# Kernel tuning notes

Hardware: AMD Instinct MI355X
Metric: run time of the kernel (lower is better)

The kernel has to match this reference:

```python
import jax, jax.numpy as jnp
import numpy as np

UNITS = 1024
B, T, F = 32, 2048, 2048  # values: [B, T, F], key dim = F // 2
DQ = 1024                 # query feature dim


def setup_inputs() -> dict:
    key = jax.random.key(0)
    k1, k2, k3, k4 = jax.random.split(key, 4)
    query = jax.random.normal(k1, (B, DQ), dtype=jnp.float32)
    values = jax.random.normal(k2, (B, T, F), dtype=jnp.float32)
    concat_dim = F // 2 + DQ  # key half concat with repeated query
    W1 = jax.random.normal(k3, (concat_dim, UNITS), dtype=jnp.float32) * (concat_dim ** -0.5)
    b1 = jnp.zeros((UNITS,), dtype=jnp.float32)
    V = jax.random.normal(k4, (UNITS, 1), dtype=jnp.float32) * (UNITS ** -0.5)
    bV = jnp.zeros((1,), dtype=jnp.float32)
    return {"query": query, "values": values, "W1": W1, "b1": b1, "V": V, "bV": bV}


def reference(query, values, W1, b1, V, bV):
    half = values.shape[2] // 2
    key = values[:, :, :half]                       # [B, T, F/2]
    # RepeatVector(query) -> [B, T, DQ]; concat with key -> [B, T, F/2 + DQ]
    s_prev = jnp.broadcast_to(query[:, None, :], (values.shape[0], values.shape[1], query.shape[1]))
    concat = jnp.concatenate([key, s_prev], axis=-1)
    e = jnp.einsum('btc,cu->btu', concat, W1) + b1   # Dense(units), no activation
    score = jnp.einsum('btu,uo->bto', e, V) + bV     # [B, T, 1]
    attention_weights = jax.nn.softmax(score, axis=1)
    # Dot(axes=1): contract time axis -> [B, 1, F]
    context_vector = jnp.einsum('bto,btf->bof', attention_weights, values)
    return (context_vector, attention_weights)
```

## Files before the change

kernel.cpp:

```cpp
#include <hip/hip_runtime.h>
#include <math.h>

#define BB 32
#define TT 2048
#define FF 2048
#define DQ 1024
#define UNITS 1024
#define HALF 1024
#define CDIM 2048
#define TC 32
#define NC (TT / TC)


__global__ void compute_w_kernel(const float* __restrict__ W1,
                                 const float* __restrict__ b1,
                                 const float* __restrict__ V,
                                 const float* __restrict__ bV,
                                 float* __restrict__ ws_w,
                                 float* __restrict__ ws_c0) {
    int g = blockIdx.x * 4 + (threadIdx.x >> 6);
    int lane = threadIdx.x & 63;
    if (g > CDIM) return;
    const float* src = (g < CDIM) ? (W1 + (size_t)g * UNITS) : b1;
    float acc = 0.f;
#pragma unroll
    for (int k = 0; k < UNITS / 256; ++k) {
        int idx = k * 256 + lane * 4;
        float4 a = *(const float4*)(src + idx);
        float4 v = *(const float4*)(V + idx);
        acc += a.x * v.x + a.y * v.y + a.z * v.z + a.w * v.w;
    }
#pragma unroll
    for (int off = 32; off >= 1; off >>= 1) acc += __shfl_down(acc, off, 64);
    if (lane == 0) {
        if (g < CDIM) ws_w[g] = acc;
        else          *ws_c0 = acc + bV[0];
    }
}

__global__ void compute_qb_kernel(const float* __restrict__ query,
                                  const float* __restrict__ ws_w,
                                  const float* __restrict__ ws_c0,
                                  float* __restrict__ ws_qb) {
    int g = blockIdx.x * 4 + (threadIdx.x >> 6);
    int lane = threadIdx.x & 63;
    if (g >= BB) return;
    const float* q = query + (size_t)g * DQ;
    const float* wq = ws_w + HALF;
    float acc = 0.f;
#pragma unroll
    for (int k = 0; k < DQ / 256; ++k) {
        int idx = k * 256 + lane * 4;
        float4 a = *(const float4*)(q + idx);
        float4 w = *(const float4*)(wq + idx);
        acc += a.x * w.x + a.y * w.y + a.z * w.z + a.w * w.w;
    }
#pragma unroll
    for (int off = 32; off >= 1; off >>= 1) acc += __shfl_down(acc, off, 64);
    if (lane == 0) ws_qb[g] = acc + *ws_c0;
}

__global__ void attn_stream_kernel(const float* __restrict__ values,
                                   const float* __restrict__ ws_w,
                                   const float* __restrict__ ws_qb,
                                   float* __restrict__ ws_scores,
                                   float* __restrict__ ws_m,
                                   float* __restrict__ ws_l,
                                   float* __restrict__ ws_ctx) {
    const int blk = blockIdx.x;
    const int b = blk / NC;
    const int chunk = blk % NC;
    const int t0 = chunk * TC;
    const int tid = threadIdx.x;
    const int lane = tid & 63;
    const int wv = tid >> 6;

    __shared__ float red[16];

    const float4 w4 = *(const float4*)(ws_w + tid * 4);
    const float qb = ws_qb[b];

    const float* vbase = values + (size_t)b * TT * FF;

    float m = -1e30f, l = 0.f;
    float4 c0 = make_float4(0.f, 0.f, 0.f, 0.f);
    float4 c1 = make_float4(0.f, 0.f, 0.f, 0.f);

    for (int r = 0; r < TC; r += 2) {
        const float* row0 = vbase + (size_t)(t0 + r) * FF;
        const float* row1 = row0 + FF;
        float4 a0 = *(const float4*)(row0 + tid * 4);
        float4 a1 = *(const float4*)(row0 + HALF + tid * 4);
        float4 e0 = *(const float4*)(row1 + tid * 4);
        float4 e1 = *(const float4*)(row1 + HALF + tid * 4);

        float pa = a0.x * w4.x + a0.y * w4.y + a0.z * w4.z + a0.w * w4.w;
        float pb = e0.x * w4.x + e0.y * w4.y + e0.z * w4.z + e0.w * w4.w;
#pragma unroll
        for (int off = 32; off >= 1; off >>= 1) {
            pa += __shfl_down(pa, off, 64);
            pb += __shfl_down(pb, off, 64);
        }
        const int par = (r >> 1) & 1;
        if (lane == 0) {
            red[par * 8 + wv * 2 + 0] = pa;
            red[par * 8 + wv * 2 + 1] = pb;
        }
        __syncthreads();
        float sa = red[par * 8 + 0] + red[par * 8 + 2] + red[par * 8 + 4] + red[par * 8 + 6] + qb;
        float sb = red[par * 8 + 1] + red[par * 8 + 3] + red[par * 8 + 5] + red[par * 8 + 7] + qb;
        if (tid == 0) {
            ws_scores[b * TT + t0 + r]     = sa;
            ws_scores[b * TT + t0 + r + 1] = sb;
        }
        {
            float mn = fmaxf(m, sa);
            float scl = __expf(m - mn);
            float p = __expf(sa - mn);
            l = l * scl + p;
            c0.x = c0.x * scl + p * a0.x; c0.y = c0.y * scl + p * a0.y;
            c0.z = c0.z * scl + p * a0.z; c0.w = c0.w * scl + p * a0.w;
            c1.x = c1.x * scl + p * a1.x; c1.y = c1.y * scl + p * a1.y;
            c1.z = c1.z * scl + p * a1.z; c1.w = c1.w * scl + p * a1.w;
            m = mn;
        }
        {
            float mn = fmaxf(m, sb);
            float scl = __expf(m - mn);
            float p = __expf(sb - mn);
            l = l * scl + p;
            c0.x = c0.x * scl + p * e0.x; c0.y = c0.y * scl + p * e0.y;
            c0.z = c0.z * scl + p * e0.z; c0.w = c0.w * scl + p * e0.w;
            c1.x = c1.x * scl + p * e1.x; c1.y = c1.y * scl + p * e1.y;
            c1.z = c1.z * scl + p * e1.z; c1.w = c1.w * scl + p * e1.w;
            m = mn;
        }
    }

    if (tid == 0) { ws_m[blk] = m; ws_l[blk] = l; }
    float* cdst = ws_ctx + (size_t)blk * FF;
    *(float4*)(cdst + tid * 4) = c0;
    *(float4*)(cdst + HALF + tid * 4) = c1;
}

__global__ void combine_kernel(const float* __restrict__ ws_scores,
                               const float* __restrict__ ws_m,
                               const float* __restrict__ ws_l,
                               const float* __restrict__ ws_ctx,
                               float* __restrict__ out) {
    const int b = blockIdx.x >> 3;
    const int seg = blockIdx.x & 7;
    const int tid = threadIdx.x;

    __shared__ float ms[NC], ls[NC];
    for (int c = tid; c < NC; c += 256) {
        ms[c] = ws_m[b * NC + c];
        ls[c] = ws_l[b * NC + c];
    }
    __syncthreads();

    float mg = -1e30f;
#pragma unroll 8
    for (int c = 0; c < NC; ++c) mg = fmaxf(mg, ms[c]);
    float lg = 0.f;
#pragma unroll 8
    for (int c = 0; c < NC; ++c) lg += ls[c] * __expf(ms[c] - mg);
    const float inv = 1.0f / lg;

    const int t = seg * 256 + tid;
    float s = ws_scores[b * TT + t];
    out[BB * FF + b * TT + t] = __expf(s - mg) * inv;

    const int f = seg * 256 + tid;
    float acc = 0.f;
#pragma unroll 8
    for (int c = 0; c < NC; ++c) {
        acc += ws_ctx[(size_t)(b * NC + c) * FF + f] * __expf(ms[c] - mg);
    }
    out[b * FF + f] = acc * inv;
}

extern "C" void kernel_launch(void* const* d_in, const int* in_sizes, int n_in,
                              void* d_out, int out_size, void* d_ws, size_t ws_size,
                              hipStream_t stream) {
    const float* query  = (const float*)d_in[0];
    const float* values = (const float*)d_in[1];
    const float* W1     = (const float*)d_in[2];
    const float* b1     = (const float*)d_in[3];
    const float* V      = (const float*)d_in[4];
    const float* bV     = (const float*)d_in[5];
    float* out = (float*)d_out;

    float* ws        = (float*)d_ws;
    float* ws_w      = ws;
    float* ws_c0     = ws + 2048;
    float* ws_qb     = ws + 2064;
    float* ws_scores = ws + 4096;
    float* ws_m      = ws + 69632;
    float* ws_l      = ws + 71680;
    float* ws_ctx    = ws + 73728;

    compute_w_kernel<<<513, 256, 0, stream>>>(W1, b1, V, bV, ws_w, ws_c0);
    compute_qb_kernel<<<8, 256, 0, stream>>>(query, ws_w, ws_c0, ws_qb);
    attn_stream_kernel<<<BB * NC, 256, 0, stream>>>(values, ws_w, ws_qb,
                                                    ws_scores, ws_m, ws_l, ws_ctx);
    combine_kernel<<<BB * 8, 256, 0, stream>>>(ws_scores, ws_m, ws_l, ws_ctx, out);
}
```

Baseline: 707.2 us.

## Assign one wavefront per time chunk with register double-buffered row loads

The streaming kernel moves from one 256-thread block per 32-row chunk to one 64-lane wavefront per 16-row chunk. Each lane holds a full row slice of 8 float4s, so the score is reduced with wave shuffles only, which removes the per-row shared-memory reduction and __syncthreads. The next row is prefetched into registers while the current one is processed, and the combine kernel precomputes per-chunk scale factors in shared memory. The trade-offs are higher register pressure (launch bounds 256,3), twice as many partial context vectors to write and reduce, and a longer combine loop.

```diff
diff --git a/kernel.cpp b/kernel.cpp
--- a/kernel.cpp
+++ b/kernel.cpp
@@ -8,7 +8,7 @@
 #define UNITS 1024
 #define HALF 1024
 #define CDIM 2048
-#define TC 32
+#define TC 16
 #define NC (TT / TC)
 
 
@@ -60,87 +60,81 @@
     if (lane == 0) ws_qb[g] = acc + *ws_c0;
 }
 
-__global__ void attn_stream_kernel(const float* __restrict__ values,
-                                   const float* __restrict__ ws_w,
-                                   const float* __restrict__ ws_qb,
-                                   float* __restrict__ ws_scores,
-                                   float* __restrict__ ws_m,
-                                   float* __restrict__ ws_l,
-                                   float* __restrict__ ws_ctx) {
-    const int blk = blockIdx.x;
-    const int b = blk / NC;
-    const int chunk = blk % NC;
-    const int t0 = chunk * TC;
-    const int tid = threadIdx.x;
-    const int lane = tid & 63;
-    const int wv = tid >> 6;
-
-    __shared__ float red[16];
-
-    const float4 w4 = *(const float4*)(ws_w + tid * 4);
+__global__ __launch_bounds__(256, 3)
+void attn_stream_kernel(const float* __restrict__ values,
+                        const float* __restrict__ ws_w,
+                        const float* __restrict__ ws_qb,
+                        float* __restrict__ ws_scores,
+                        float* __restrict__ ws_m,
+                        float* __restrict__ ws_l,
+                        float* __restrict__ ws_ctx) {
+    const int lane = threadIdx.x & 63;
+    const int wv   = threadIdx.x >> 6;
+    const int g    = blockIdx.x * 4 + wv;
+    const int b    = g >> 7;
+    const int chunk= g & (NC - 1);
+    const int t0   = chunk * TC;
+
+    const float4 w0 = *(const float4*)(ws_w + 0 * 256 + lane * 4);
+    const float4 w1 = *(const float4*)(ws_w + 1 * 256 + lane * 4);
+    const float4 w2 = *(const float4*)(ws_w + 2 * 256 + lane * 4);
+    const float4 w3 = *(const float4*)(ws_w + 3 * 256 + lane * 4);
     const float qb = ws_qb[b];
 
-    const float* vbase = values + (size_t)b * TT * FF;
-
-    float m = -1e30f, l = 0.f;
-    float4 c0 = make_float4(0.f, 0.f, 0.f, 0.f);
-    float4 c1 = make_float4(0.f, 0.f, 0.f, 0.f);
-
+    const float* vbase = values + (size_t)b * TT * FF + (size_t)t0 * FF + lane * 4;
+
+    float4 acc[8];
+#pragma unroll
+    for (int j = 0; j < 8; ++j) acc[j] = make_float4(0.f, 0.f, 0.f, 0.f);
+
+    float m = -1e30f, l = 0.f, skeep = 0.f;
+
+    float4 va[8], vb[8];
+#pragma unroll
+    for (int j = 0; j < 8; ++j) va[j] = *(const float4*)(vbase + j * 256);
+
+    auto process = [&](const float4 (&v)[8], int ri) {
+        float d = v[0].x * w0.x + v[0].y * w0.y + v[0].z * w0.z + v[0].w * w0.w
+                + v[1].x * w1.x + v[1].y * w1.y + v[1].z * w1.z + v[1].w * w1.w
+                + v[2].x * w2.x + v[2].y * w2.y + v[2].z * w2.z + v[2].w * w2.w
+                + v[3].x * w3.x + v[3].y * w3.y + v[3].z * w3.z + v[3].w * w3.w;
+#pragma unroll
+        for (int off = 1; off <= 32; off <<= 1) d += __shfl_xor(d, off, 64);
+        const float s = d + qb;
+        skeep = (lane == ri) ? s : skeep;
+        const float mn  = fmaxf(m, s);
+        const float scl = __expf(m - mn);
+        const float p   = __expf(s - mn);
+        l = l * scl + p;
+#pragma unroll
+        for (int j = 0; j < 8; ++j) {
+            acc[j].x = acc[j].x * scl + p * v[j].x;
+            acc[j].y = acc[j].y * scl + p * v[j].y;
+            acc[j].z = acc[j].z * scl + p * v[j].z;
+            acc[j].w = acc[j].w * scl + p * v[j].w;
+        }
+        m = mn;
+    };
+
+#pragma unroll
     for (int r = 0; r < TC; r += 2) {
-        const float* row0 = vbase + (size_t)(t0 + r) * FF;
-        const float* row1 = row0 + FF;
-        float4 a0 = *(const float4*)(row0 + tid * 4);
-        float4 a1 = *(const float4*)(row0 + HALF + tid * 4);
-        float4 e0 = *(const float4*)(row1 + tid * 4);
-        float4 e1 = *(const float4*)(row1 + HALF + tid * 4);
-
-        float pa = a0.x * w4.x + a0.y * w4.y + a0.z * w4.z + a0.w * w4.w;
-        float pb = e0.x * w4.x + e0.y * w4.y + e0.z * w4.z + e0.w * w4.w;
-#pragma unroll
-        for (int off = 32; off >= 1; off >>= 1) {
-            pa += __shfl_down(pa, off, 64);
-            pb += __shfl_down(pb, off, 64);
+        const float* rb = vbase + (size_t)(r + 1) * FF;
+#pragma unroll
+        for (int j = 0; j < 8; ++j) vb[j] = *(const float4*)(rb + j * 256);
+        process(va, r);
+        if (r + 2 < TC) {
+            const float* ra = vbase + (size_t)(r + 2) * FF;
+#pragma unroll
+            for (int j = 0; j < 8; ++j) va[j] = *(const float4*)(ra + j * 256);
         }
-        const int par = (r >> 1) & 1;
-        if (lane == 0) {
-            red[par * 8 + wv * 2 + 0] = pa;
-            red[par * 8 + wv * 2 + 1] = pb;
-        }
-        __syncthreads();
-        float sa = red[par * 8 + 0] + red[par * 8 + 2] + red[par * 8 + 4] + red[par * 8 + 6] + qb;
-        float sb = red[par * 8 + 1] + red[par * 8 + 3] + red[par * 8 + 5] + red[par * 8 + 7] + qb;
-        if (tid == 0) {
-            ws_scores[b * TT + t0 + r]     = sa;
-            ws_scores[b * TT + t0 + r + 1] = sb;
-        }
-        {
-            float mn = fmaxf(m, sa);
-            float scl = __expf(m - mn);
-            float p = __expf(sa - mn);
-            l = l * scl + p;
-            c0.x = c0.x * scl + p * a0.x; c0.y = c0.y * scl + p * a0.y;
-            c0.z = c0.z * scl + p * a0.z; c0.w = c0.w * scl + p * a0.w;
-            c1.x = c1.x * scl + p * a1.x; c1.y = c1.y * scl + p * a1.y;
-            c1.z = c1.z * scl + p * a1.z; c1.w = c1.w * scl + p * a1.w;
-            m = mn;
-        }
-        {
-            float mn = fmaxf(m, sb);
-            float scl = __expf(m - mn);
-            float p = __expf(sb - mn);
-            l = l * scl + p;
-            c0.x = c0.x * scl + p * e0.x; c0.y = c0.y * scl + p * e0.y;
-            c0.z = c0.z * scl + p * e0.z; c0.w = c0.w * scl + p * e0.w;
-            c1.x = c1.x * scl + p * e1.x; c1.y = c1.y * scl + p * e1.y;
-            c1.z = c1.z * scl + p * e1.z; c1.w = c1.w * scl + p * e1.w;
-            m = mn;
-        }
-    }
-
-    if (tid == 0) { ws_m[blk] = m; ws_l[blk] = l; }
-    float* cdst = ws_ctx + (size_t)blk * FF;
-    *(float4*)(cdst + tid * 4) = c0;
-    *(float4*)(cdst + HALF + tid * 4) = c1;
+        process(vb, r + 1);
+    }
+
+    if (lane < TC) ws_scores[b * TT + t0 + lane] = skeep;
+    if (lane == 0) { ws_m[g] = m; ws_l[g] = l; }
+    float* cdst = ws_ctx + (size_t)g * FF + lane * 4;
+#pragma unroll
+    for (int j = 0; j < 8; ++j) *(float4*)(cdst + j * 256) = acc[j];
 }
 
 __global__ void combine_kernel(const float* __restrict__ ws_scores,
@@ -152,7 +146,7 @@
     const int seg = blockIdx.x & 7;
     const int tid = threadIdx.x;
 
-    __shared__ float ms[NC], ls[NC];
+    __shared__ float ms[NC], ls[NC], co[NC];
     for (int c = tid; c < NC; c += 256) {
         ms[c] = ws_m[b * NC + c];
         ls[c] = ws_l[b * NC + c];
@@ -167,17 +161,19 @@
     for (int c = 0; c < NC; ++c) lg += ls[c] * __expf(ms[c] - mg);
     const float inv = 1.0f / lg;
 
+    for (int c = tid; c < NC; c += 256) co[c] = __expf(ms[c] - mg) * inv;
+    __syncthreads();
+
     const int t = seg * 256 + tid;
-    float s = ws_scores[b * TT + t];
-    out[BB * FF + b * TT + t] = __expf(s - mg) * inv;
+    out[BB * FF + b * TT + t] = __expf(ws_scores[b * TT + t] - mg) * inv;
 
     const int f = seg * 256 + tid;
     float acc = 0.f;
 #pragma unroll 8
     for (int c = 0; c < NC; ++c) {
-        acc += ws_ctx[(size_t)(b * NC + c) * FF + f] * __expf(ms[c] - mg);
-    }
-    out[b * FF + f] = acc * inv;
+        acc += ws_ctx[(size_t)(b * NC + c) * FF + f] * co[c];
+    }
+    out[b * FF + f] = acc;
 }
 
 extern "C" void kernel_launch(void* const* d_in, const int* in_sizes, int n_in,
@@ -197,12 +193,12 @@
     float* ws_qb     = ws + 2064;
     float* ws_scores = ws + 4096;
     float* ws_m      = ws + 69632;
-    float* ws_l      = ws + 71680;
-    float* ws_ctx    = ws + 73728;
+    float* ws_l      = ws + 73728;
+    float* ws_ctx    = ws + 81920;
 
     compute_w_kernel<<<513, 256, 0, stream>>>(W1, b1, V, bV, ws_w, ws_c0);
     compute_qb_kernel<<<8, 256, 0, stream>>>(query, ws_w, ws_c0, ws_qb);
-    attn_stream_kernel<<<BB * NC, 256, 0, stream>>>(values, ws_w, ws_qb,
-                                                    ws_scores, ws_m, ws_l, ws_ctx);
+    attn_stream_kernel<<<(BB * NC) / 4, 256, 0, stream>>>(values, ws_w, ws_qb,
+                                                          ws_scores, ws_m, ws_l, ws_ctx);
     combine_kernel<<<BB * 8, 256, 0, stream>>>(ws_scores, ws_m, ws_l, ws_ctx, out);
 }
```

Result: slower. 1.029 ms (+45.5%).
